# Optimization experiments

Measured on AMD Instinct MI355X. Metric: run time of the kernel, lower is better.

The kernel has to match this reference:

```python
import jax, jax.numpy as jnp
import numpy as np

NORM_RADIUS = 5.0
SPATIAL_SCALE = 1.0
USE_DISKS = False
INVALID_FILL = 1e6


def setup_inputs() -> dict:
    key = jax.random.key(0)
    k1, k2, k3 = jax.random.split(key, 3)
    B, C, H, W = 8, 3, 512, 512
    P2 = 48  # 2 groups (pos/neg) x 24 clicks each
    x = jax.random.normal(k1, (B, C, H, W), dtype=jnp.float32)
    xy = jax.random.uniform(k2, (B, P2, 2), dtype=jnp.float32, minval=0.0, maxval=512.0)
    valid = jax.random.uniform(k3, (B, P2, 1)) < 0.9
    xy = jnp.where(valid, xy, -1.0)
    coords = jnp.concatenate([xy, jnp.zeros((B, P2, 1), jnp.float32)], axis=2)
    return {"x": x, "coords": coords}


def reference(x, coords):
    rows, cols = x.shape[2], x.shape[3]
    B, P2, _ = coords.shape
    P = P2 // 2  # clicks per group
    pts = coords[..., :2].reshape(-1, 2)              # [N, 2] (row, col), N = B*P2
    invalid = jnp.max(pts, axis=1) < 0                # flagged before scaling (as in torch)
    pts = pts * SPATIAL_SCALE
    rr = jnp.arange(rows, dtype=jnp.float32)[:, None]  # [rows, 1]
    cc = jnp.arange(cols, dtype=jnp.float32)[None, :]  # [1, cols]
    scale = NORM_RADIUS * SPATIAL_SCALE
    dr = rr[None, :, :] - pts[:, 0][:, None, None]     # [N, rows, cols]
    dc = cc[None, :, :] - pts[:, 1][:, None, None]
    if not USE_DISKS:
        dr = dr / scale
        dc = dc / scale
    d2 = dr * dr + dc * dc                             # squared distance map per point
    d2 = jnp.where(invalid[:, None, None], INVALID_FILL, d2)
    d2 = d2.reshape(B * 2, P, rows, cols).min(axis=1)  # min over clicks in each group
    if USE_DISKS:
        out = (d2 <= scale ** 2).astype(jnp.float32)
    else:
        out = jnp.tanh(2.0 * jnp.sqrt(d2))
    return out.reshape(B, 2, rows, cols)
```

## Files before the change

### kernel.cpp

```cpp
#include <hip/hip_runtime.h>

#define HH 512
#define WW 512
#define PP 24
#define NPT 48
#define TH 16
#define TW 64
#define RCUT2 256.0f

__device__ __forceinline__ float tanh2sqrt(float m) {
    float s = __builtin_amdgcn_sqrtf(m);
    float e = __expf(-4.0f * s);
    return __fdividef(1.0f - e, 1.0f + e);
}

__global__ __launch_bounds__(256) void DistMaps_37434934952233_kernel(
    const float* __restrict__ coords, float* __restrict__ out)
{
    const int blk  = blockIdx.x;
    const int map  = blk >> 8;
    const int tile = blk & 255;
    const int r0   = (tile >> 3) << 4;
    const int c0   = (tile & 7) << 6;
    const int b    = map >> 1;
    const int g    = map & 1;

    constexpr float INV_SCALE = 1.0f / 5.0f;

    __shared__ float npr[PP];
    __shared__ float npc[PP];
    __shared__ int   nnear;

    const int t = threadIdx.x;
    if (t == 0) nnear = 0;
    __syncthreads();

    if (t < PP) {
        const float* cp = coords + (size_t)(b * NPT + g * PP + t) * 3;
        const float pr = cp[0];
        const float pc = cp[1];
        const bool valid = fmaxf(pr, pc) >= 0.0f;
        const float dr = fmaxf(0.0f, fmaxf((float)r0 - pr, pr - (float)(r0 + TH - 1)));
        const float dc = fmaxf(0.0f, fmaxf((float)c0 - pc, pc - (float)(c0 + TW - 1)));
        if (valid && (dr * dr + dc * dc) <= RCUT2) {
            const int i = atomicAdd(&nnear, 1);
            npr[i] = pr * INV_SCALE;
            npc[i] = pc * INV_SCALE;
        }
    }
    __syncthreads();

    const int r  = r0 + (t >> 4);
    const int cc = c0 + ((t & 15) << 2);
    const int n  = nnear;

    float4 o;
    if (n == 0) {
        o.x = 1.0f; o.y = 1.0f; o.z = 1.0f; o.w = 1.0f;
    } else {
        const float rs  = (float)r  * INV_SCALE;
        const float cs0 = (float)cc * INV_SCALE;
        const float cs1 = cs0 + INV_SCALE;
        const float cs2 = cs0 + 2.0f * INV_SCALE;
        const float cs3 = cs0 + 3.0f * INV_SCALE;

        float m0 = 1e30f, m1 = 1e30f, m2 = 1e30f, m3 = 1e30f;
        for (int p = 0; p < n; ++p) {
            const float pr = npr[p];
            const float pc = npc[p];
            const float dr  = rs - pr;
            const float dr2 = dr * dr;
            float d;
            d = cs0 - pc; m0 = fminf(m0, fmaf(d, d, dr2));
            d = cs1 - pc; m1 = fminf(m1, fmaf(d, d, dr2));
            d = cs2 - pc; m2 = fminf(m2, fmaf(d, d, dr2));
            d = cs3 - pc; m3 = fminf(m3, fmaf(d, d, dr2));
        }
        o.x = tanh2sqrt(m0);
        o.y = tanh2sqrt(m1);
        o.z = tanh2sqrt(m2);
        o.w = tanh2sqrt(m3);
    }

    const size_t idx = ((size_t)map * HH + r) * WW + cc;
    *reinterpret_cast<float4*>(out + idx) = o;
}

extern "C" void kernel_launch(void* const* d_in, const int* in_sizes, int n_in,
                              void* d_out, int out_size, void* d_ws, size_t ws_size,
                              hipStream_t stream) {
    (void)in_sizes; (void)n_in; (void)d_ws; (void)ws_size; (void)out_size;
    const float* coords = (const float*)d_in[1];
    float* out = (float*)d_out;
    DistMaps_37434934952233_kernel<<<16 * 256, 256, 0, stream>>>(coords, out);
}
```

Before: 73.11 us.

## Enlarge tiles to 32x128 with 4 rows per thread and ballot-based culling

Each block now covers a 32x128 tile, and each thread computes 4 rows by 4 columns, reusing the column distance terms across rows. The shared-memory atomic compaction of near points is replaced by a wavefront ballot and popcount prefix, which removes one barrier. Larger tiles mean fewer blocks and less per-block setup, but more points pass the cull for each tile, and the 1024-block grid may lower occupancy on a large GPU.

```diff
diff --git a/kernel.cpp b/kernel.cpp
--- a/kernel.cpp
+++ b/kernel.cpp
@@ -4,8 +4,8 @@
 #define WW 512
 #define PP 24
 #define NPT 48
-#define TH 16
-#define TW 64
+#define TH 32
+#define TW 128
 #define RCUT2 256.0f
 
 __device__ __forceinline__ float tanh2sqrt(float m) {
@@ -18,10 +18,10 @@
     const float* __restrict__ coords, float* __restrict__ out)
 {
     const int blk  = blockIdx.x;
-    const int map  = blk >> 8;
-    const int tile = blk & 255;
-    const int r0   = (tile >> 3) << 4;
-    const int c0   = (tile & 7) << 6;
+    const int map  = blk >> 6;
+    const int tile = blk & 63;
+    const int r0   = (tile >> 2) << 5;
+    const int c0   = (tile & 3) << 7;
     const int b    = map >> 1;
     const int g    = map & 1;
 
@@ -32,58 +32,83 @@
     __shared__ int   nnear;
 
     const int t = threadIdx.x;
-    if (t == 0) nnear = 0;
-    __syncthreads();
 
-    if (t < PP) {
-        const float* cp = coords + (size_t)(b * NPT + g * PP + t) * 3;
-        const float pr = cp[0];
-        const float pc = cp[1];
-        const bool valid = fmaxf(pr, pc) >= 0.0f;
-        const float dr = fmaxf(0.0f, fmaxf((float)r0 - pr, pr - (float)(r0 + TH - 1)));
-        const float dc = fmaxf(0.0f, fmaxf((float)c0 - pc, pc - (float)(c0 + TW - 1)));
-        if (valid && (dr * dr + dc * dc) <= RCUT2) {
-            const int i = atomicAdd(&nnear, 1);
+    if (t < 64) {
+        bool near = false;
+        float pr = 0.0f, pc = 0.0f;
+        if (t < PP) {
+            const float* cp = coords + (size_t)(b * NPT + g * PP + t) * 3;
+            pr = cp[0];
+            pc = cp[1];
+            const bool valid = fmaxf(pr, pc) >= 0.0f;
+            const float dr = fmaxf(0.0f, fmaxf((float)r0 - pr, pr - (float)(r0 + TH - 1)));
+            const float dc = fmaxf(0.0f, fmaxf((float)c0 - pc, pc - (float)(c0 + TW - 1)));
+            near = valid && (dr * dr + dc * dc) <= RCUT2;
+        }
+        const unsigned long long m = __ballot(near);
+        if (near) {
+            const int i = __popcll(m & ((1ull << t) - 1ull));
             npr[i] = pr * INV_SCALE;
             npc[i] = pc * INV_SCALE;
         }
+        if (t == 0) nnear = (int)__popcll(m);
     }
     __syncthreads();
 
-    const int r  = r0 + (t >> 4);
-    const int cc = c0 + ((t & 15) << 2);
+    const int rb = r0 + (t >> 5);
+    const int cc = c0 + ((t & 31) << 2);
     const int n  = nnear;
 
-    float4 o;
+    float* op = out + ((size_t)map * HH + rb) * WW + cc;
+
     if (n == 0) {
-        o.x = 1.0f; o.y = 1.0f; o.z = 1.0f; o.w = 1.0f;
-    } else {
-        const float rs  = (float)r  * INV_SCALE;
-        const float cs0 = (float)cc * INV_SCALE;
-        const float cs1 = cs0 + INV_SCALE;
-        const float cs2 = cs0 + 2.0f * INV_SCALE;
-        const float cs3 = cs0 + 3.0f * INV_SCALE;
-
-        float m0 = 1e30f, m1 = 1e30f, m2 = 1e30f, m3 = 1e30f;
-        for (int p = 0; p < n; ++p) {
-            const float pr = npr[p];
-            const float pc = npc[p];
-            const float dr  = rs - pr;
-            const float dr2 = dr * dr;
-            float d;
-            d = cs0 - pc; m0 = fminf(m0, fmaf(d, d, dr2));
-            d = cs1 - pc; m1 = fminf(m1, fmaf(d, d, dr2));
-            d = cs2 - pc; m2 = fminf(m2, fmaf(d, d, dr2));
-            d = cs3 - pc; m3 = fminf(m3, fmaf(d, d, dr2));
-        }
-        o.x = tanh2sqrt(m0);
-        o.y = tanh2sqrt(m1);
-        o.z = tanh2sqrt(m2);
-        o.w = tanh2sqrt(m3);
+        const float4 one = make_float4(1.0f, 1.0f, 1.0f, 1.0f);
+        #pragma unroll
+        for (int k = 0; k < 4; ++k)
+            *reinterpret_cast<float4*>(op + (size_t)k * 8 * WW) = one;
+        return;
     }
 
-    const size_t idx = ((size_t)map * HH + r) * WW + cc;
-    *reinterpret_cast<float4*>(out + idx) = o;
+    const float cs0 = (float)cc * INV_SCALE;
+    const float cs1 = cs0 + INV_SCALE;
+    const float cs2 = cs0 + 2.0f * INV_SCALE;
+    const float cs3 = cs0 + 3.0f * INV_SCALE;
+
+    float rs[4];
+    #pragma unroll
+    for (int k = 0; k < 4; ++k) rs[k] = (float)(rb + 8 * k) * INV_SCALE;
+
+    float mm[4][4];
+    #pragma unroll
+    for (int k = 0; k < 4; ++k)
+        #pragma unroll
+        for (int j = 0; j < 4; ++j) mm[k][j] = 1e30f;
+
+    for (int p = 0; p < n; ++p) {
+        const float pr = npr[p];
+        const float pc = npc[p];
+        const float d0 = cs0 - pc, d1 = cs1 - pc, d2 = cs2 - pc, d3 = cs3 - pc;
+        const float e0 = d0 * d0, e1 = d1 * d1, e2 = d2 * d2, e3 = d3 * d3;
+        #pragma unroll
+        for (int k = 0; k < 4; ++k) {
+            const float dr  = rs[k] - pr;
+            const float dr2 = dr * dr;
+            mm[k][0] = fminf(mm[k][0], e0 + dr2);
+            mm[k][1] = fminf(mm[k][1], e1 + dr2);
+            mm[k][2] = fminf(mm[k][2], e2 + dr2);
+            mm[k][3] = fminf(mm[k][3], e3 + dr2);
+        }
+    }
+
+    #pragma unroll
+    for (int k = 0; k < 4; ++k) {
+        float4 o;
+        o.x = tanh2sqrt(mm[k][0]);
+        o.y = tanh2sqrt(mm[k][1]);
+        o.z = tanh2sqrt(mm[k][2]);
+        o.w = tanh2sqrt(mm[k][3]);
+        *reinterpret_cast<float4*>(op + (size_t)k * 8 * WW) = o;
+    }
 }
 
 extern "C" void kernel_launch(void* const* d_in, const int* in_sizes, int n_in,
@@ -92,5 +117,5 @@
     (void)in_sizes; (void)n_in; (void)d_ws; (void)ws_size; (void)out_size;
     const float* coords = (const float*)d_in[1];
     float* out = (float*)d_out;
-    DistMaps_37434934952233_kernel<<<16 * 256, 256, 0, stream>>>(coords, out);
+    DistMaps_37434934952233_kernel<<<16 * 64, 256, 0, stream>>>(coords, out);
 }
```

New measurement: 74.68 us. +2.2%, slower.
